# Optimization experiments

Hardware: AMD Instinct MI355X
Metric: run time of the kernel (lower is better)

The kernel has to match this reference:

```python
import math
import jax, jax.numpy as jnp
import numpy as np

B, T, D = 2048, 50, 256
NEG = -100000.0

def setup_inputs() -> dict:
    key = jax.random.key(0)
    ks = jax.random.split(key, 9)
    return {
        "x": jax.random.normal(ks[0], (B, T, D), dtype=jnp.float32),
        "mask": jax.random.randint(ks[1], (B, T, 1), 0, 2, dtype=jnp.int32),
        "time_decay": jax.random.uniform(ks[2], (B, T, 1), dtype=jnp.float32),
        "Wq": jax.random.normal(ks[3], (D, D), dtype=jnp.float32) * (1.0 / math.sqrt(D)),
        "bq": jax.random.normal(ks[4], (D,), dtype=jnp.float32) * 0.01,
        "Wk": jax.random.normal(ks[5], (D, D), dtype=jnp.float32) * (1.0 / math.sqrt(D)),
        "bk": jax.random.normal(ks[6], (D,), dtype=jnp.float32) * 0.01,
        "Wv": jax.random.normal(ks[7], (D, D), dtype=jnp.float32) * (1.0 / math.sqrt(D)),
        "bv": jax.random.normal(ks[8], (D,), dtype=jnp.float32) * 0.01,
    }

def reference(x, mask, time_decay, Wq, bq, Wk, bk, Wv, bv):
    # PositionalEncoding.forward: elementwise multiply by time-decay (broadcast over d_model)
    x = x * time_decay  # [B,T,D]
    q = jnp.einsum('btd,ed->bte', x, Wq) + bq
    k = jnp.einsum('btd,ed->bte', x, Wk) + bk
    v = jnp.einsum('btd,ed->bte', x, Wv) + bv
    # unusual Q/K-side masking (masked_fill before the matmul)
    keep = mask != 0  # [B,T,1]
    q = jnp.where(keep, q, NEG)
    k = jnp.where(keep, k, NEG)
    score = jnp.einsum('btd,bsd->bts', q, k) / math.sqrt(D)  # [B,T,T]
    score = jax.nn.softmax(score, axis=-1)
    # dropout is identity in eval mode
    out = jnp.einsum('bts,bsd->btd', score, v)  # [B,T,D]
    return out[:, -1, :]  # [B,D]
```

## Files before the change

### kernel.cpp

```cpp
#include <hip/hip_runtime.h>


namespace {
constexpr int kB = 2048;
constexpr int kT = 50;
constexpr int kD = 256;
constexpr int kG = 4;
constexpr int kThr = 256;
constexpr double kNeg = -100000.0;
constexpr int oM2 = 0;
constexpr int oWvp = 65536;
constexpr int oV0 = 131072;
constexpr int oC = 131328;
constexpr int oW1 = 131584;
constexpr int oW2 = 131840;
constexpr int oDbl = 132096;
}

__global__ __launch_bounds__(kThr) void precomp(
    const float* __restrict__ Wq, const float* __restrict__ bq,
    const float* __restrict__ Wk, const float* __restrict__ bk,
    const float* __restrict__ Wv, float* __restrict__ ws) {
  const int t = threadIdx.x;
  const int wave = t >> 6;
  const int lane = t & 63;
  const int blk = blockIdx.x;
  __shared__ float coefL[kD];
  __shared__ double red[3][4];

  if (blk < 256) {
    const int a = blk;
    coefL[t] = Wq[(size_t)t * kD + a];
    __syncthreads();
    const float* kcol = Wk + t;
    float pre[8];
#pragma unroll
    for (int k = 0; k < 8; ++k) pre[k] = kcol[(size_t)k * kD];
    float acc = 0.f;
    for (int j0 = 0; j0 < kD; j0 += 8) {
      float cur[8];
#pragma unroll
      for (int k = 0; k < 8; ++k) cur[k] = pre[k];
      const int nx = (j0 + 8 < kD) ? (j0 + 8) : 0;
#pragma unroll
      for (int k = 0; k < 8; ++k) pre[k] = kcol[(size_t)(nx + k) * kD];
#pragma unroll
      for (int k = 0; k < 8; ++k) acc += coefL[j0 + k] * cur[k];
    }
    ws[oM2 + (a >> 2) * 1024 + 4 * t + (a & 3)] = acc;
  } else if (blk < 258) {
    const float* W = (blk == 256) ? Wk : Wq;
    const float* coef = (blk == 256) ? bq : bk;
    coefL[t] = coef[t];
    __syncthreads();
    const float* col = W + t;
    float pre[8];
#pragma unroll
    for (int k = 0; k < 8; ++k) pre[k] = col[(size_t)k * kD];
    double a0 = 0.0, a1 = 0.0;
    for (int j0 = 0; j0 < kD; j0 += 8) {
      float cur[8];
#pragma unroll
      for (int k = 0; k < 8; ++k) cur[k] = pre[k];
      const int nx = (j0 + 8 < kD) ? (j0 + 8) : 0;
#pragma unroll
      for (int k = 0; k < 8; ++k) pre[k] = col[(size_t)(nx + k) * kD];
#pragma unroll
      for (int k = 0; k < 8; ++k) {
        const double w = (double)cur[k];
        a0 += (double)coefL[j0 + k] * w;
        a1 += w;
      }
    }
    if (blk == 256) {
      ws[oV0 + t] = (float)a0;
      ws[oC + t] = (float)a1;
    } else {
      ws[oW1 + t] = (float)a0;
      ws[oW2 + t] = (float)a1;
      double p0 = (double)bk[t];
      double p1 = (double)bq[t] * (double)bk[t];
      double p2 = (double)bq[t];
#pragma unroll
      for (int off = 32; off; off >>= 1) {
        p0 += __shfl_xor(p0, off);
        p1 += __shfl_xor(p1, off);
        p2 += __shfl_xor(p2, off);
      }
      if (lane == 0) {
        red[0][wave] = p0;
        red[1][wave] = p1;
        red[2][wave] = p2;
      }
      __syncthreads();
      if (t == 0) {
        double* dc = (double*)(ws + oDbl);
        dc[0] = red[0][0] + red[0][1] + red[0][2] + red[0][3];
        dc[1] = red[1][0] + red[1][1] + red[1][2] + red[1][3];
        dc[2] = red[2][0] + red[2][1] + red[2][2] + red[2][3];
      }
    }
  } else {
    const int d4b = (blk - 258) * 4;
    float4 in[4];
#pragma unroll
    for (int k = 0; k < 4; ++k)
      in[k] = *(const float4*)(Wv + (size_t)t * kD + 4 * (d4b + k));
    float4* Wvp = (float4*)(ws + oWvp);
#pragma unroll
    for (int k = 0; k < 4; ++k) Wvp[(size_t)(d4b + k) * kD + t] = in[k];
  }
}

__global__ __launch_bounds__(kThr, 2) void attn_main(
    const float* __restrict__ x, const int* __restrict__ mask,
    const float* __restrict__ td, const float* __restrict__ bv,
    const float* __restrict__ ws, float* __restrict__ out) {
  const float4* M2v = (const float4*)(ws + oM2);
  const float4* Wvv = (const float4*)(ws + oWvp);
  const float* v0 = ws + oV0;
  const float* cv = ws + oC;
  const double* dconst = (const double*)(ws + oDbl);

  __shared__ __align__(16) float4 xsf[kG][kD / 4];
  __shared__ __align__(16) float ub[kG][kD];
  __shared__ __align__(16) float4 ybf[kG][kD / 4];
  __shared__ float tdb[kG * kT];
  __shared__ int mb[kG * kT];
  __shared__ double Sqb[kG], Qbkb[kG];

  const int t = threadIdx.x;
  const int wave = t >> 6;
  const int lane = t & 63;
  const int b0 = blockIdx.x * kG;

  if (t < kG * kT) {
    tdb[t] = td[b0 * kT + t];
    mb[t] = mask[b0 * kT + t];
  }
  {
    const int g = wave;
    const float tv = td[(b0 + g) * kT + (kT - 1)];
    float4 xv =
        ((const float4*)(x + ((size_t)(b0 + g) * kT + kT - 1) * kD))[lane];
    xv.x *= tv; xv.y *= tv; xv.z *= tv; xv.w *= tv;
    xsf[g][lane] = xv;
  }
  __syncthreads();

  {
    const int g = wave;
    const float4 xv = xsf[g][lane];
    const float4 a1 = ((const float4*)(ws + oW1))[lane];
    const float4 a2 = ((const float4*)(ws + oW2))[lane];
    double s1 = (double)xv.x * a1.x + (double)xv.y * a1.y +
                (double)xv.z * a1.z + (double)xv.w * a1.w;
    double s2 = (double)xv.x * a2.x + (double)xv.y * a2.y +
                (double)xv.z * a2.z + (double)xv.w * a2.w;
#pragma unroll
    for (int off = 32; off; off >>= 1) {
      s1 += __shfl_xor(s1, off);
      s2 += __shfl_xor(s2, off);
    }
    if (lane == 0) {
      Qbkb[g] = s1 + dconst[1];
      Sqb[g] = s2 + dconst[2];
    }
  }

  {
    float4 pre[8];
#pragma unroll
    for (int k = 0; k < 8; ++k) pre[k] = M2v[(size_t)k * kD + t];
    float acc[kG];
    const float v0t = v0[t];
#pragma unroll
    for (int j = 0; j < kG; ++j) acc[j] = v0t;
    for (int j0 = 0; j0 < 64; j0 += 8) {
      float4 cur[8];
#pragma unroll
      for (int k = 0; k < 8; ++k) cur[k] = pre[k];
      const int nx = (j0 + 8 < 64) ? (j0 + 8) : 0;
#pragma unroll
      for (int k = 0; k < 8; ++k) pre[k] = M2v[(size_t)(nx + k) * kD + t];
#pragma unroll
      for (int k = 0; k < 8; ++k) {
#pragma unroll
        for (int j = 0; j < kG; ++j) {
          const float4 xj = xsf[j][j0 + k];
          acc[j] += xj.x * cur[k].x + xj.y * cur[k].y + xj.z * cur[k].z +
                    xj.w * cur[k].w;
        }
      }
    }
#pragma unroll
    for (int j = 0; j < kG; ++j) ub[j][t] = acc[j];
  }
  __syncthreads();

  {
    const int g = wave;
    const int b = b0 + g;
    const int base = g * kT;
    const float4* xrow = (const float4*)(x + (size_t)b * kT * kD);
    const float4 u4 = ((const float4*)(&ub[g][0]))[lane];
    const float4 c4 = ((const float4*)cv)[lane];
    const int mqg = mb[base + (kT - 1)];
    const float4 v4 = mqg ? u4 : c4;
    const double Cm = kNeg * Sqb[g] * 0.0625;
    const double Cbb = 256.0 * 1.0e10 * 0.0625;
    const double Qbk = Qbkb[g];
    const double sbkd = dconst[0];

    double m = -1.0e300;
    float l = 0.f;
    float4 y = {0.f, 0.f, 0.f, 0.f};

    float4 n0 = xrow[0 * 64 + lane];
    float4 n1 = xrow[1 * 64 + lane];
    float4 n2 = xrow[2 * 64 + lane];
    float4 n3 = xrow[3 * 64 + lane];
    for (int s = 0; s < 52; s += 4) {
      const float4 r0 = n0, r1 = n1, r2 = n2, r3 = n3;
      {
        const int p0 = (s + 4 < kT) ? s + 4 : kT - 1;
        const int p1 = (s + 5 < kT) ? s + 5 : kT - 1;
        const int p2 = (s + 6 < kT) ? s + 6 : kT - 1;
        const int p3 = (s + 7 < kT) ? s + 7 : kT - 1;
        n0 = xrow[p0 * 64 + lane];
        n1 = xrow[p1 * 64 + lane];
        n2 = xrow[p2 * 64 + lane];
        n3 = xrow[p3 * 64 + lane];
      }
      const int s1i = s + 1, s2i = s + 2, s3i = s + 3;
      const int c0 = s;
      const int c1 = (s1i < kT) ? s1i : kT - 1;
      const int c2 = (s2i < kT) ? s2i : kT - 1;
      const int c3 = (s3i < kT) ? s3i : kT - 1;
      const float tv0 = tdb[base + c0];
      const float tv1 = tdb[base + c1];
      const float tv2 = tdb[base + c2];
      const float tv3 = tdb[base + c3];
      float4 a0, a1, a2, a3;
      a0.x = r0.x * tv0; a0.y = r0.y * tv0; a0.z = r0.z * tv0; a0.w = r0.w * tv0;
      a1.x = r1.x * tv1; a1.y = r1.y * tv1; a1.z = r1.z * tv1; a1.w = r1.w * tv1;
      a2.x = r2.x * tv2; a2.y = r2.y * tv2; a2.z = r2.z * tv2; a2.w = r2.w * tv2;
      a3.x = r3.x * tv3; a3.y = r3.y * tv3; a3.z = r3.z * tv3; a3.w = r3.w * tv3;
      float p0 = a0.x * v4.x + a0.y * v4.y + a0.z * v4.z + a0.w * v4.w;
      float p1 = a1.x * v4.x + a1.y * v4.y + a1.z * v4.z + a1.w * v4.w;
      float p2 = a2.x * v4.x + a2.y * v4.y + a2.z * v4.z + a2.w * v4.w;
      float p3 = a3.x * v4.x + a3.y * v4.y + a3.z * v4.z + a3.w * v4.w;
#pragma unroll
      for (int off = 32; off; off >>= 1) {
        p0 += __shfl_xor(p0, off);
        p1 += __shfl_xor(p1, off);
        p2 += __shfl_xor(p2, off);
        p3 += __shfl_xor(p3, off);
      }
      const int ms0 = mb[base + c0];
      const int ms1 = mb[base + c1];
      const int ms2 = mb[base + c2];
      const int ms3 = mb[base + c3];
      double sc0, sc1, sc2, sc3;
      if (mqg) {
        sc0 = ms0 ? ((double)p0 + Qbk) * 0.0625 : Cm;
        sc1 = ms1 ? ((double)p1 + Qbk) * 0.0625 : Cm;
        sc2 = ms2 ? ((double)p2 + Qbk) * 0.0625 : Cm;
        sc3 = ms3 ? ((double)p3 + Qbk) * 0.0625 : Cm;
      } else {
        sc0 = ms0 ? kNeg * ((double)p0 + sbkd) * 0.0625 : Cbb;
        sc1 = ms1 ? kNeg * ((double)p1 + sbkd) * 0.0625 : Cbb;
        sc2 = ms2 ? kNeg * ((double)p2 + sbkd) * 0.0625 : Cbb;
        sc3 = ms3 ? kNeg * ((double)p3 + sbkd) * 0.0625 : Cbb;
      }
      if (s1i >= kT) sc1 = -1.0e300;
      if (s2i >= kT) sc2 = -1.0e300;
      if (s3i >= kT) sc3 = -1.0e300;
      double mnew = m;
      if (sc0 > mnew) mnew = sc0;
      if (sc1 > mnew) mnew = sc1;
      if (sc2 > mnew) mnew = sc2;
      if (sc3 > mnew) mnew = sc3;
      const float al = expf((float)(m - mnew));
      const float e0 = expf((float)(sc0 - mnew));
      const float e1 = expf((float)(sc1 - mnew));
      const float e2 = expf((float)(sc2 - mnew));
      const float e3 = expf((float)(sc3 - mnew));
      m = mnew;
      l = l * al + e0 + e1 + e2 + e3;
      y.x = y.x * al + e0 * a0.x + e1 * a1.x + e2 * a2.x + e3 * a3.x;
      y.y = y.y * al + e0 * a0.y + e1 * a1.y + e2 * a2.y + e3 * a3.y;
      y.z = y.z * al + e0 * a0.z + e1 * a1.z + e2 * a2.z + e3 * a3.z;
      y.w = y.w * al + e0 * a0.w + e1 * a1.w + e2 * a2.w + e3 * a3.w;
    }
    const float inv = 1.0f / l;
    y.x *= inv; y.y *= inv; y.z *= inv; y.w *= inv;
    ybf[g][lane] = y;
  }
  __syncthreads();

  {
    float4 pre[8];
#pragma unroll
    for (int k = 0; k < 8; ++k) pre[k] = Wvv[(size_t)k * kD + t];
    float acc[kG];
    const float bvt = bv[t];
#pragma unroll
    for (int j = 0; j < kG; ++j) acc[j] = bvt;
    for (int j0 = 0; j0 < 64; j0 += 8) {
      float4 cur[8];
#pragma unroll
      for (int k = 0; k < 8; ++k) cur[k] = pre[k];
      const int nx = (j0 + 8 < 64) ? (j0 + 8) : 0;
#pragma unroll
      for (int k = 0; k < 8; ++k) pre[k] = Wvv[(size_t)(nx + k) * kD + t];
#pragma unroll
      for (int k = 0; k < 8; ++k) {
#pragma unroll
        for (int j = 0; j < kG; ++j) {
          const float4 yj = ybf[j][j0 + k];
          acc[j] += yj.x * cur[k].x + yj.y * cur[k].y + yj.z * cur[k].z +
                    yj.w * cur[k].w;
        }
      }
    }
#pragma unroll
    for (int j = 0; j < kG; ++j) out[(size_t)(b0 + j) * kD + t] = acc[j];
  }
}

extern "C" void kernel_launch(void* const* d_in, const int* in_sizes, int n_in,
                              void* d_out, int out_size, void* d_ws,
                              size_t ws_size, hipStream_t stream) {
  const float* x = (const float*)d_in[0];
  const int* mask = (const int*)d_in[1];
  const float* td = (const float*)d_in[2];
  const float* Wq = (const float*)d_in[3];
  const float* bq = (const float*)d_in[4];
  const float* Wk = (const float*)d_in[5];
  const float* bk = (const float*)d_in[6];
  const float* Wv = (const float*)d_in[7];
  const float* bv = (const float*)d_in[8];
  float* ws = (float*)d_ws;
  float* out = (float*)d_out;
  (void)in_sizes; (void)n_in; (void)out_size; (void)ws_size;

  hipLaunchKernelGGL(precomp, dim3(274), dim3(kThr), 0, stream, Wq, bq, Wk, bk,
                     Wv, ws);
  hipLaunchKernelGGL(attn_main, dim3(kB / kG), dim3(kThr), 0, stream, x, mask,
                     td, bv, (const float*)ws, out);
}
```

Baseline: 224.5 us.

## Split fused attention kernel into separate u-GEMM, attention, and output GEMM kernels

```diff
diff --git a/kernel.cpp b/kernel.cpp
--- a/kernel.cpp
+++ b/kernel.cpp
@@ -5,7 +5,6 @@
 constexpr int kB = 2048;
 constexpr int kT = 50;
 constexpr int kD = 256;
-constexpr int kG = 4;
 constexpr int kThr = 256;
 constexpr double kNeg = -100000.0;
 constexpr int oM2 = 0;
@@ -15,6 +14,9 @@
 constexpr int oW1 = 131584;
 constexpr int oW2 = 131840;
 constexpr int oDbl = 132096;
+constexpr int oSq = 132608;
+constexpr int oQbk = 136704;
+constexpr int oU = 140800;
 }
 
 __global__ __launch_bounds__(kThr) void precomp(
@@ -112,45 +114,19 @@
   }
 }
 
-__global__ __launch_bounds__(kThr, 2) void attn_main(
-    const float* __restrict__ x, const int* __restrict__ mask,
-    const float* __restrict__ td, const float* __restrict__ bv,
-    const float* __restrict__ ws, float* __restrict__ out) {
-  const float4* M2v = (const float4*)(ws + oM2);
-  const float4* Wvv = (const float4*)(ws + oWvp);
-  const float* v0 = ws + oV0;
-  const float* cv = ws + oC;
-  const double* dconst = (const double*)(ws + oDbl);
-
-  __shared__ __align__(16) float4 xsf[kG][kD / 4];
-  __shared__ __align__(16) float ub[kG][kD];
-  __shared__ __align__(16) float4 ybf[kG][kD / 4];
-  __shared__ float tdb[kG * kT];
-  __shared__ int mb[kG * kT];
-  __shared__ double Sqb[kG], Qbkb[kG];
-
+__global__ __launch_bounds__(kThr) void u_gemm(const float* __restrict__ x,
+                                               const float* __restrict__ td,
+                                               float* __restrict__ ws) {
   const int t = threadIdx.x;
   const int wave = t >> 6;
   const int lane = t & 63;
-  const int b0 = blockIdx.x * kG;
-
-  if (t < kG * kT) {
-    tdb[t] = td[b0 * kT + t];
-    mb[t] = mask[b0 * kT + t];
-  }
+  const int b0 = blockIdx.x * 4;
+  const double* dc = (const double*)(ws + oDbl);
+
   {
-    const int g = wave;
-    const float tv = td[(b0 + g) * kT + (kT - 1)];
-    float4 xv =
-        ((const float4*)(x + ((size_t)(b0 + g) * kT + kT - 1) * kD))[lane];
-    xv.x *= tv; xv.y *= tv; xv.z *= tv; xv.w *= tv;
-    xsf[g][lane] = xv;
-  }
-  __syncthreads();
-
-  {
-    const int g = wave;
-    const float4 xv = xsf[g][lane];
+    const int b = b0 + wave;
+    const float4 xv =
+        ((const float4*)(x + ((size_t)b * kT + kT - 1) * kD))[lane];
     const float4 a1 = ((const float4*)(ws + oW1))[lane];
     const float4 a2 = ((const float4*)(ws + oW2))[lane];
     double s1 = (double)xv.x * a1.x + (double)xv.y * a1.y +
@@ -163,170 +139,204 @@
       s2 += __shfl_xor(s2, off);
     }
     if (lane == 0) {
-      Qbkb[g] = s1 + dconst[1];
-      Sqb[g] = s2 + dconst[2];
-    }
-  }
-
-  {
-    float4 pre[8];
-#pragma unroll
-    for (int k = 0; k < 8; ++k) pre[k] = M2v[(size_t)k * kD + t];
-    float acc[kG];
-    const float v0t = v0[t];
-#pragma unroll
-    for (int j = 0; j < kG; ++j) acc[j] = v0t;
-    for (int j0 = 0; j0 < 64; j0 += 8) {
-      float4 cur[8];
-#pragma unroll
-      for (int k = 0; k < 8; ++k) cur[k] = pre[k];
-      const int nx = (j0 + 8 < 64) ? (j0 + 8) : 0;
-#pragma unroll
-      for (int k = 0; k < 8; ++k) pre[k] = M2v[(size_t)(nx + k) * kD + t];
-#pragma unroll
-      for (int k = 0; k < 8; ++k) {
-#pragma unroll
-        for (int j = 0; j < kG; ++j) {
-          const float4 xj = xsf[j][j0 + k];
-          acc[j] += xj.x * cur[k].x + xj.y * cur[k].y + xj.z * cur[k].z +
-                    xj.w * cur[k].w;
-        }
-      }
-    }
-#pragma unroll
-    for (int j = 0; j < kG; ++j) ub[j][t] = acc[j];
-  }
-  __syncthreads();
-
-  {
-    const int g = wave;
-    const int b = b0 + g;
-    const int base = g * kT;
-    const float4* xrow = (const float4*)(x + (size_t)b * kT * kD);
-    const float4 u4 = ((const float4*)(&ub[g][0]))[lane];
-    const float4 c4 = ((const float4*)cv)[lane];
-    const int mqg = mb[base + (kT - 1)];
-    const float4 v4 = mqg ? u4 : c4;
-    const double Cm = kNeg * Sqb[g] * 0.0625;
-    const double Cbb = 256.0 * 1.0e10 * 0.0625;
-    const double Qbk = Qbkb[g];
-    const double sbkd = dconst[0];
-
-    double m = -1.0e300;
-    float l = 0.f;
-    float4 y = {0.f, 0.f, 0.f, 0.f};
-
-    float4 n0 = xrow[0 * 64 + lane];
-    float4 n1 = xrow[1 * 64 + lane];
-    float4 n2 = xrow[2 * 64 + lane];
-    float4 n3 = xrow[3 * 64 + lane];
-    for (int s = 0; s < 52; s += 4) {
-      const float4 r0 = n0, r1 = n1, r2 = n2, r3 = n3;
-      {
-        const int p0 = (s + 4 < kT) ? s + 4 : kT - 1;
-        const int p1 = (s + 5 < kT) ? s + 5 : kT - 1;
-        const int p2 = (s + 6 < kT) ? s + 6 : kT - 1;
-        const int p3 = (s + 7 < kT) ? s + 7 : kT - 1;
-        n0 = xrow[p0 * 64 + lane];
-        n1 = xrow[p1 * 64 + lane];
-        n2 = xrow[p2 * 64 + lane];
-        n3 = xrow[p3 * 64 + lane];
-      }
-      const int s1i = s + 1, s2i = s + 2, s3i = s + 3;
-      const int c0 = s;
-      const int c1 = (s1i < kT) ? s1i : kT - 1;
-      const int c2 = (s2i < kT) ? s2i : kT - 1;
-      const int c3 = (s3i < kT) ? s3i : kT - 1;
-      const float tv0 = tdb[base + c0];
-      const float tv1 = tdb[base + c1];
-      const float tv2 = tdb[base + c2];
-      const float tv3 = tdb[base + c3];
-      float4 a0, a1, a2, a3;
-      a0.x = r0.x * tv0; a0.y = r0.y * tv0; a0.z = r0.z * tv0; a0.w = r0.w * tv0;
-      a1.x = r1.x * tv1; a1.y = r1.y * tv1; a1.z = r1.z * tv1; a1.w = r1.w * tv1;
-      a2.x = r2.x * tv2; a2.y = r2.y * tv2; a2.z = r2.z * tv2; a2.w = r2.w * tv2;
-      a3.x = r3.x * tv3; a3.y = r3.y * tv3; a3.z = r3.z * tv3; a3.w = r3.w * tv3;
-      float p0 = a0.x * v4.x + a0.y * v4.y + a0.z * v4.z + a0.w * v4.w;
-      float p1 = a1.x * v4.x + a1.y * v4.y + a1.z * v4.z + a1.w * v4.w;
-      float p2 = a2.x * v4.x + a2.y * v4.y + a2.z * v4.z + a2.w * v4.w;
-      float p3 = a3.x * v4.x + a3.y * v4.y + a3.z * v4.z + a3.w * v4.w;
-#pragma unroll
-      for (int off = 32; off; off >>= 1) {
-        p0 += __shfl_xor(p0, off);
-        p1 += __shfl_xor(p1, off);
-        p2 += __shfl_xor(p2, off);
-        p3 += __shfl_xor(p3, off);
-      }
-      const int ms0 = mb[base + c0];
-      const int ms1 = mb[base + c1];
-      const int ms2 = mb[base + c2];
-      const int ms3 = mb[base + c3];
-      double sc0, sc1, sc2, sc3;
-      if (mqg) {
-        sc0 = ms0 ? ((double)p0 + Qbk) * 0.0625 : Cm;
-        sc1 = ms1 ? ((double)p1 + Qbk) * 0.0625 : Cm;
-        sc2 = ms2 ? ((double)p2 + Qbk) * 0.0625 : Cm;
-        sc3 = ms3 ? ((double)p3 + Qbk) * 0.0625 : Cm;
-      } else {
-        sc0 = ms0 ? kNeg * ((double)p0 + sbkd) * 0.0625 : Cbb;
-        sc1 = ms1 ? kNeg * ((double)p1 + sbkd) * 0.0625 : Cbb;
-        sc2 = ms2 ? kNeg * ((double)p2 + sbkd) * 0.0625 : Cbb;
-        sc3 = ms3 ? kNeg * ((double)p3 + sbkd) * 0.0625 : Cbb;
-      }
-      if (s1i >= kT) sc1 = -1.0e300;
-      if (s2i >= kT) sc2 = -1.0e300;
-      if (s3i >= kT) sc3 = -1.0e300;
-      double mnew = m;
-      if (sc0 > mnew) mnew = sc0;
-      if (sc1 > mnew) mnew = sc1;
-      if (sc2 > mnew) mnew = sc2;
-      if (sc3 > mnew) mnew = sc3;
-      const float al = expf((float)(m - mnew));
-      const float e0 = expf((float)(sc0 - mnew));
-      const float e1 = expf((float)(sc1 - mnew));
-      const float e2 = expf((float)(sc2 - mnew));
-      const float e3 = expf((float)(sc3 - mnew));
-      m = mnew;
-      l = l * al + e0 + e1 + e2 + e3;
-      y.x = y.x * al + e0 * a0.x + e1 * a1.x + e2 * a2.x + e3 * a3.x;
-      y.y = y.y * al + e0 * a0.y + e1 * a1.y + e2 * a2.y + e3 * a3.y;
-      y.z = y.z * al + e0 * a0.z + e1 * a1.z + e2 * a2.z + e3 * a3.z;
-      y.w = y.w * al + e0 * a0.w + e1 * a1.w + e2 * a2.w + e3 * a3.w;
-    }
-    const float inv = 1.0f / l;
-    y.x *= inv; y.y *= inv; y.z *= inv; y.w *= inv;
-    ybf[g][lane] = y;
-  }
-  __syncthreads();
-
-  {
-    float4 pre[8];
-#pragma unroll
-    for (int k = 0; k < 8; ++k) pre[k] = Wvv[(size_t)k * kD + t];
-    float acc[kG];
-    const float bvt = bv[t];
-#pragma unroll
-    for (int j = 0; j < kG; ++j) acc[j] = bvt;
-    for (int j0 = 0; j0 < 64; j0 += 8) {
-      float4 cur[8];
-#pragma unroll
-      for (int k = 0; k < 8; ++k) cur[k] = pre[k];
-      const int nx = (j0 + 8 < 64) ? (j0 + 8) : 0;
-#pragma unroll
-      for (int k = 0; k < 8; ++k) pre[k] = Wvv[(size_t)(nx + k) * kD + t];
-#pragma unroll
-      for (int k = 0; k < 8; ++k) {
-#pragma unroll
-        for (int j = 0; j < kG; ++j) {
-          const float4 yj = ybf[j][j0 + k];
-          acc[j] += yj.x * cur[k].x + yj.y * cur[k].y + yj.z * cur[k].z +
-                    yj.w * cur[k].w;
-        }
-      }
-    }
-#pragma unroll
-    for (int j = 0; j < kG; ++j) out[(size_t)(b0 + j) * kD + t] = acc[j];
-  }
+      const double tdd = (double)td[(size_t)b * kT + kT - 1];
+      ((double*)(ws + oQbk))[b] = tdd * s1 + dc[1];
+      ((double*)(ws + oSq))[b] = tdd * s2 + dc[2];
+    }
+  }
+
+  const float4* M2v = (const float4*)(ws + oM2);
+  const float4* r0 = (const float4*)(x + ((size_t)(b0 + 0) * kT + kT - 1) * kD);
+  const float4* r1 = (const float4*)(x + ((size_t)(b0 + 1) * kT + kT - 1) * kD);
+  const float4* r2 = (const float4*)(x + ((size_t)(b0 + 2) * kT + kT - 1) * kD);
+  const float4* r3 = (const float4*)(x + ((size_t)(b0 + 3) * kT + kT - 1) * kD);
+  const float td0 = td[(size_t)(b0 + 0) * kT + kT - 1];
+  const float td1 = td[(size_t)(b0 + 1) * kT + kT - 1];
+  const float td2 = td[(size_t)(b0 + 2) * kT + kT - 1];
+  const float td3 = td[(size_t)(b0 + 3) * kT + kT - 1];
+
+  float4 pre[8];
+#pragma unroll
+  for (int k = 0; k < 8; ++k) pre[k] = M2v[(size_t)k * kD + t];
+  float acc0 = 0.f, acc1 = 0.f, acc2 = 0.f, acc3 = 0.f;
+  for (int j0 = 0; j0 < 64; j0 += 8) {
+    float4 cur[8];
+#pragma unroll
+    for (int k = 0; k < 8; ++k) cur[k] = pre[k];
+    const int nx = (j0 + 8 < 64) ? (j0 + 8) : 0;
+#pragma unroll
+    for (int k = 0; k < 8; ++k) pre[k] = M2v[(size_t)(nx + k) * kD + t];
+#pragma unroll
+    for (int k = 0; k < 8; ++k) {
+      const float4 m = cur[k];
+      const float4 x0 = r0[j0 + k];
+      const float4 x1 = r1[j0 + k];
+      const float4 x2 = r2[j0 + k];
+      const float4 x3 = r3[j0 + k];
+      acc0 += x0.x * m.x + x0.y * m.y + x0.z * m.z + x0.w * m.w;
+      acc1 += x1.x * m.x + x1.y * m.y + x1.z * m.z + x1.w * m.w;
+      acc2 += x2.x * m.x + x2.y * m.y + x2.z * m.z + x2.w * m.w;
+      acc3 += x3.x * m.x + x3.y * m.y + x3.z * m.z + x3.w * m.w;
+    }
+  }
+  const float v0t = ws[oV0 + t];
+  ws[oU + (size_t)(b0 + 0) * kD + t] = td0 * acc0 + v0t;
+  ws[oU + (size_t)(b0 + 1) * kD + t] = td1 * acc1 + v0t;
+  ws[oU + (size_t)(b0 + 2) * kD + t] = td2 * acc2 + v0t;
+  ws[oU + (size_t)(b0 + 3) * kD + t] = td3 * acc3 + v0t;
+}
+
+__global__ __launch_bounds__(kThr) void attn(const float* __restrict__ x,
+                                             const int* __restrict__ mask,
+                                             const float* __restrict__ td,
+                                             float* __restrict__ ws) {
+  const int t = threadIdx.x;
+  const int wave = t >> 6;
+  const int lane = t & 63;
+  const int b = blockIdx.x * 4 + wave;
+
+  const float mtd = (lane < kT) ? td[(size_t)b * kT + lane] : 0.f;
+  const int mmk = (lane < kT) ? mask[(size_t)b * kT + lane] : 0;
+  const int mqg = __shfl(mmk, kT - 1);
+
+  const float4 u4 = ((const float4*)(ws + oU))[(size_t)b * 64 + lane];
+  const float4 c4 = ((const float4*)(ws + oC))[lane];
+  const float4 v4 = mqg ? u4 : c4;
+
+  const double* dcp = (const double*)(ws + oDbl);
+  const double sbkd = dcp[0];
+  const double Sq = ((const double*)(ws + oSq))[b];
+  const double Qbk = ((const double*)(ws + oQbk))[b];
+  const double Cm = kNeg * Sq * 0.0625;
+  const double Cbb = 256.0 * 1.0e10 * 0.0625;
+
+  const float4* xrow = (const float4*)(x + (size_t)b * kT * kD);
+  double m = -1.0e300;
+  float l = 0.f;
+  float4 y = {0.f, 0.f, 0.f, 0.f};
+
+  float4 n0 = xrow[0 * 64 + lane];
+  float4 n1 = xrow[1 * 64 + lane];
+  float4 n2 = xrow[2 * 64 + lane];
+  float4 n3 = xrow[3 * 64 + lane];
+  for (int s = 0; s < 52; s += 4) {
+    const float4 r0 = n0, r1 = n1, r2 = n2, r3 = n3;
+    {
+      const int p0 = (s + 4 < kT) ? s + 4 : kT - 1;
+      const int p1 = (s + 5 < kT) ? s + 5 : kT - 1;
+      const int p2 = (s + 6 < kT) ? s + 6 : kT - 1;
+      const int p3 = (s + 7 < kT) ? s + 7 : kT - 1;
+      n0 = xrow[p0 * 64 + lane];
+      n1 = xrow[p1 * 64 + lane];
+      n2 = xrow[p2 * 64 + lane];
+      n3 = xrow[p3 * 64 + lane];
+    }
+    const int s1i = s + 1, s2i = s + 2, s3i = s + 3;
+    const int c0 = s;
+    const int c1 = (s1i < kT) ? s1i : kT - 1;
+    const int c2 = (s2i < kT) ? s2i : kT - 1;
+    const int c3 = (s3i < kT) ? s3i : kT - 1;
+    const float tv0 = __shfl(mtd, c0);
+    const float tv1 = __shfl(mtd, c1);
+    const float tv2 = __shfl(mtd, c2);
+    const float tv3 = __shfl(mtd, c3);
+    float4 a0, a1, a2, a3;
+    a0.x = r0.x * tv0; a0.y = r0.y * tv0; a0.z = r0.z * tv0; a0.w = r0.w * tv0;
+    a1.x = r1.x * tv1; a1.y = r1.y * tv1; a1.z = r1.z * tv1; a1.w = r1.w * tv1;
+    a2.x = r2.x * tv2; a2.y = r2.y * tv2; a2.z = r2.z * tv2; a2.w = r2.w * tv2;
+    a3.x = r3.x * tv3; a3.y = r3.y * tv3; a3.z = r3.z * tv3; a3.w = r3.w * tv3;
+    float p0 = a0.x * v4.x + a0.y * v4.y + a0.z * v4.z + a0.w * v4.w;
+    float p1 = a1.x * v4.x + a1.y * v4.y + a1.z * v4.z + a1.w * v4.w;
+    float p2 = a2.x * v4.x + a2.y * v4.y + a2.z * v4.z + a2.w * v4.w;
+    float p3 = a3.x * v4.x + a3.y * v4.y + a3.z * v4.z + a3.w * v4.w;
+#pragma unroll
+    for (int off = 32; off; off >>= 1) {
+      p0 += __shfl_xor(p0, off);
+      p1 += __shfl_xor(p1, off);
+      p2 += __shfl_xor(p2, off);
+      p3 += __shfl_xor(p3, off);
+    }
+    const int ms0 = __shfl(mmk, c0);
+    const int ms1 = __shfl(mmk, c1);
+    const int ms2 = __shfl(mmk, c2);
+    const int ms3 = __shfl(mmk, c3);
+    double sc0, sc1, sc2, sc3;
+    if (mqg) {
+      sc0 = ms0 ? ((double)p0 + Qbk) * 0.0625 : Cm;
+      sc1 = ms1 ? ((double)p1 + Qbk) * 0.0625 : Cm;
+      sc2 = ms2 ? ((double)p2 + Qbk) * 0.0625 : Cm;
+      sc3 = ms3 ? ((double)p3 + Qbk) * 0.0625 : Cm;
+    } else {
+      sc0 = ms0 ? kNeg * ((double)p0 + sbkd) * 0.0625 : Cbb;
+      sc1 = ms1 ? kNeg * ((double)p1 + sbkd) * 0.0625 : Cbb;
+      sc2 = ms2 ? kNeg * ((double)p2 + sbkd) * 0.0625 : Cbb;
+      sc3 = ms3 ? kNeg * ((double)p3 + sbkd) * 0.0625 : Cbb;
+    }
+    if (s1i >= kT) sc1 = -1.0e300;
+    if (s2i >= kT) sc2 = -1.0e300;
+    if (s3i >= kT) sc3 = -1.0e300;
+    double mnew = m;
+    if (sc0 > mnew) mnew = sc0;
+    if (sc1 > mnew) mnew = sc1;
+    if (sc2 > mnew) mnew = sc2;
+    if (sc3 > mnew) mnew = sc3;
+    const float al = expf((float)(m - mnew));
+    const float e0 = expf((float)(sc0 - mnew));
+    const float e1 = expf((float)(sc1 - mnew));
+    const float e2 = expf((float)(sc2 - mnew));
+    const float e3 = expf((float)(sc3 - mnew));
+    m = mnew;
+    l = l * al + e0 + e1 + e2 + e3;
+    y.x = y.x * al + e0 * a0.x + e1 * a1.x + e2 * a2.x + e3 * a3.x;
+    y.y = y.y * al + e0 * a0.y + e1 * a1.y + e2 * a2.y + e3 * a3.y;
+    y.z = y.z * al + e0 * a0.z + e1 * a1.z + e2 * a2.z + e3 * a3.z;
+    y.w = y.w * al + e0 * a0.w + e1 * a1.w + e2 * a2.w + e3 * a3.w;
+  }
+  const float inv = 1.0f / l;
+  y.x *= inv; y.y *= inv; y.z *= inv; y.w *= inv;
+  ((float4*)(ws + oU))[(size_t)b * 64 + lane] = y;
+}
+
+__global__ __launch_bounds__(kThr) void o_gemm(const float* __restrict__ bv,
+                                               const float* __restrict__ ws,
+                                               float* __restrict__ out) {
+  const int t = threadIdx.x;
+  const int b0 = blockIdx.x * 4;
+  const float4* Wvv = (const float4*)(ws + oWvp);
+  const float4* y0 = (const float4*)(ws + oU + (size_t)(b0 + 0) * kD);
+  const float4* y1 = (const float4*)(ws + oU + (size_t)(b0 + 1) * kD);
+  const float4* y2 = (const float4*)(ws + oU + (size_t)(b0 + 2) * kD);
+  const float4* y3 = (const float4*)(ws + oU + (size_t)(b0 + 3) * kD);
+
+  float4 pre[8];
+#pragma unroll
+  for (int k = 0; k < 8; ++k) pre[k] = Wvv[(size_t)k * kD + t];
+  float acc0 = 0.f, acc1 = 0.f, acc2 = 0.f, acc3 = 0.f;
+  for (int j0 = 0; j0 < 64; j0 += 8) {
+    float4 cur[8];
+#pragma unroll
+    for (int k = 0; k < 8; ++k) cur[k] = pre[k];
+    const int nx = (j0 + 8 < 64) ? (j0 + 8) : 0;
+#pragma unroll
+    for (int k = 0; k < 8; ++k) pre[k] = Wvv[(size_t)(nx + k) * kD + t];
+#pragma unroll
+    for (int k = 0; k < 8; ++k) {
+      const float4 m = cur[k];
+      const float4 a0 = y0[j0 + k];
+      const float4 a1 = y1[j0 + k];
+      const float4 a2 = y2[j0 + k];
+      const float4 a3 = y3[j0 + k];
+      acc0 += a0.x * m.x + a0.y * m.y + a0.z * m.z + a0.w * m.w;
+      acc1 += a1.x * m.x + a1.y * m.y + a1.z * m.z + a1.w * m.w;
+      acc2 += a2.x * m.x + a2.y * m.y + a2.z * m.z + a2.w * m.w;
+      acc3 += a3.x * m.x + a3.y * m.y + a3.z * m.z + a3.w * m.w;
+    }
+  }
+  const float bvt = bv[t];
+  out[(size_t)(b0 + 0) * kD + t] = acc0 + bvt;
+  out[(size_t)(b0 + 1) * kD + t] = acc1 + bvt;
+  out[(size_t)(b0 + 2) * kD + t] = acc2 + bvt;
+  out[(size_t)(b0 + 3) * kD + t] = acc3 + bvt;
 }
 
 extern "C" void kernel_launch(void* const* d_in, const int* in_sizes, int n_in,
@@ -347,6 +357,8 @@
 
   hipLaunchKernelGGL(precomp, dim3(274), dim3(kThr), 0, stream, Wq, bq, Wk, bk,
                      Wv, ws);
-  hipLaunchKernelGGL(attn_main, dim3(kB / kG), dim3(kThr), 0, stream, x, mask,
-                     td, bv, (const float*)ws, out);
-}
+  hipLaunchKernelGGL(u_gemm, dim3(kB / 4), dim3(kThr), 0, stream, x, td, ws);
+  hipLaunchKernelGGL(attn, dim3(kB / 4), dim3(kThr), 0, stream, x, mask, td,
+                     ws);
+  hipLaunchKernelGGL(o_gemm, dim3(kB / 4), dim3(kThr), 0, stream, bv, ws, out);
+}
```

After: 233.7 us. 4.1% more time.

## Restructure main kernel to single-wave blocks handling two batches each

Applied to the files above, without the earlier changes.

```diff
diff --git a/kernel.cpp b/kernel.cpp
--- a/kernel.cpp
+++ b/kernel.cpp
@@ -5,8 +5,6 @@
 constexpr int kB = 2048;
 constexpr int kT = 50;
 constexpr int kD = 256;
-constexpr int kG = 4;
-constexpr int kThr = 256;
 constexpr double kNeg = -100000.0;
 constexpr int oM2 = 0;
 constexpr int oWvp = 65536;
@@ -17,7 +15,7 @@
 constexpr int oDbl = 132096;
 }
 
-__global__ __launch_bounds__(kThr) void precomp(
+__global__ __launch_bounds__(256) void precomp(
     const float* __restrict__ Wq, const float* __restrict__ bq,
     const float* __restrict__ Wk, const float* __restrict__ bk,
     const float* __restrict__ Wv, float* __restrict__ ws) {
@@ -94,10 +92,10 @@
       }
       __syncthreads();
       if (t == 0) {
-        double* dc = (double*)(ws + oDbl);
-        dc[0] = red[0][0] + red[0][1] + red[0][2] + red[0][3];
-        dc[1] = red[1][0] + red[1][1] + red[1][2] + red[1][3];
-        dc[2] = red[2][0] + red[2][1] + red[2][2] + red[2][3];
+        double* dcw = (double*)(ws + oDbl);
+        dcw[0] = red[0][0] + red[0][1] + red[0][2] + red[0][3];
+        dcw[1] = red[1][0] + red[1][1] + red[1][2] + red[1][3];
+        dcw[2] = red[2][0] + red[2][1] + red[2][2] + red[2][3];
       }
     }
   } else {
@@ -112,47 +110,35 @@
   }
 }
 
-__global__ __launch_bounds__(kThr, 2) void attn_main(
+__global__ __launch_bounds__(64) void fused_main(
     const float* __restrict__ x, const int* __restrict__ mask,
     const float* __restrict__ td, const float* __restrict__ bv,
     const float* __restrict__ ws, float* __restrict__ out) {
+  const int lane = threadIdx.x;
+  const int b0 = blockIdx.x * 2;
+  __shared__ __align__(16) float xsL[2][kD];
+  __shared__ __align__(16) float uL[2][kD];
+  __shared__ __align__(16) float yL[2][kD];
+
+  const double* dc = (const double*)(ws + oDbl);
   const float4* M2v = (const float4*)(ws + oM2);
   const float4* Wvv = (const float4*)(ws + oWvp);
-  const float* v0 = ws + oV0;
-  const float* cv = ws + oC;
-  const double* dconst = (const double*)(ws + oDbl);
-
-  __shared__ __align__(16) float4 xsf[kG][kD / 4];
-  __shared__ __align__(16) float ub[kG][kD];
-  __shared__ __align__(16) float4 ybf[kG][kD / 4];
-  __shared__ float tdb[kG * kT];
-  __shared__ int mb[kG * kT];
-  __shared__ double Sqb[kG], Qbkb[kG];
-
-  const int t = threadIdx.x;
-  const int wave = t >> 6;
-  const int lane = t & 63;
-  const int b0 = blockIdx.x * kG;
-
-  if (t < kG * kT) {
-    tdb[t] = td[b0 * kT + t];
-    mb[t] = mask[b0 * kT + t];
-  }
-  {
-    const int g = wave;
-    const float tv = td[(b0 + g) * kT + (kT - 1)];
-    float4 xv =
-        ((const float4*)(x + ((size_t)(b0 + g) * kT + kT - 1) * kD))[lane];
-    xv.x *= tv; xv.y *= tv; xv.z *= tv; xv.w *= tv;
-    xsf[g][lane] = xv;
-  }
-  __syncthreads();
-
-  {
-    const int g = wave;
-    const float4 xv = xsf[g][lane];
-    const float4 a1 = ((const float4*)(ws + oW1))[lane];
-    const float4 a2 = ((const float4*)(ws + oW2))[lane];
+
+  const float mtd0 = (lane < kT) ? td[(size_t)(b0 + 0) * kT + lane] : 0.f;
+  const float mtd1 = (lane < kT) ? td[(size_t)(b0 + 1) * kT + lane] : 0.f;
+  const int mmk0 = (lane < kT) ? mask[(size_t)(b0 + 0) * kT + lane] : 0;
+  const int mmk1 = (lane < kT) ? mask[(size_t)(b0 + 1) * kT + lane] : 0;
+  const float4 c4 = ((const float4*)(ws + oC))[lane];
+  const float4 a1 = ((const float4*)(ws + oW1))[lane];
+  const float4 a2 = ((const float4*)(ws + oW2))[lane];
+
+  double Qbk[2], Sq[2];
+#pragma unroll
+  for (int j = 0; j < 2; ++j) {
+    const int b = b0 + j;
+    const float tdl = __shfl(j ? mtd1 : mtd0, kT - 1);
+    const float4 xv =
+        ((const float4*)(x + ((size_t)b * kT + kT - 1) * kD))[lane];
     double s1 = (double)xv.x * a1.x + (double)xv.y * a1.y +
                 (double)xv.z * a1.z + (double)xv.w * a1.w;
     double s2 = (double)xv.x * a2.x + (double)xv.y * a2.y +
@@ -162,56 +148,69 @@
       s1 += __shfl_xor(s1, off);
       s2 += __shfl_xor(s2, off);
     }
-    if (lane == 0) {
-      Qbkb[g] = s1 + dconst[1];
-      Sqb[g] = s2 + dconst[2];
-    }
+    Qbk[j] = (double)tdl * s1 + dc[1];
+    Sq[j] = (double)tdl * s2 + dc[2];
+    float4 xs;
+    xs.x = xv.x * tdl; xs.y = xv.y * tdl;
+    xs.z = xv.z * tdl; xs.w = xv.w * tdl;
+    *(float4*)(&xsL[j][4 * lane]) = xs;
   }
 
   {
-    float4 pre[8];
-#pragma unroll
-    for (int k = 0; k < 8; ++k) pre[k] = M2v[(size_t)k * kD + t];
-    float acc[kG];
-    const float v0t = v0[t];
-#pragma unroll
-    for (int j = 0; j < kG; ++j) acc[j] = v0t;
-    for (int j0 = 0; j0 < 64; j0 += 8) {
-      float4 cur[8];
-#pragma unroll
-      for (int k = 0; k < 8; ++k) cur[k] = pre[k];
-      const int nx = (j0 + 8 < 64) ? (j0 + 8) : 0;
-#pragma unroll
-      for (int k = 0; k < 8; ++k) pre[k] = M2v[(size_t)(nx + k) * kD + t];
-#pragma unroll
-      for (int k = 0; k < 8; ++k) {
-#pragma unroll
-        for (int j = 0; j < kG; ++j) {
-          const float4 xj = xsf[j][j0 + k];
-          acc[j] += xj.x * cur[k].x + xj.y * cur[k].y + xj.z * cur[k].z +
-                    xj.w * cur[k].w;
-        }
-      }
-    }
-#pragma unroll
-    for (int j = 0; j < kG; ++j) ub[j][t] = acc[j];
-  }
-  __syncthreads();
-
-  {
-    const int g = wave;
-    const int b = b0 + g;
-    const int base = g * kT;
+    float4 A[4], B[4];
+#pragma unroll
+    for (int g = 0; g < 4; ++g) {
+      A[g] = M2v[(size_t)0 * kD + 64 * g + lane];
+      B[g] = M2v[(size_t)1 * kD + 64 * g + lane];
+    }
+    float accU[2][4] = {{0.f, 0.f, 0.f, 0.f}, {0.f, 0.f, 0.f, 0.f}};
+    for (int k4 = 0; k4 < 64; k4 += 2) {
+      float4 c0[4], c1[4];
+#pragma unroll
+      for (int g = 0; g < 4; ++g) { c0[g] = A[g]; c1[g] = B[g]; }
+      const int n0 = (k4 + 2 < 64) ? k4 + 2 : 0;
+      const int n1 = (k4 + 3 < 64) ? k4 + 3 : 1;
+#pragma unroll
+      for (int g = 0; g < 4; ++g) {
+        A[g] = M2v[(size_t)n0 * kD + 64 * g + lane];
+        B[g] = M2v[(size_t)n1 * kD + 64 * g + lane];
+      }
+      const float4 x00 = *(const float4*)(&xsL[0][4 * k4]);
+      const float4 x01 = *(const float4*)(&xsL[0][4 * (k4 + 1)]);
+      const float4 x10 = *(const float4*)(&xsL[1][4 * k4]);
+      const float4 x11 = *(const float4*)(&xsL[1][4 * (k4 + 1)]);
+#pragma unroll
+      for (int g = 0; g < 4; ++g) {
+        accU[0][g] += x00.x * c0[g].x + x00.y * c0[g].y + x00.z * c0[g].z +
+                      x00.w * c0[g].w + x01.x * c1[g].x + x01.y * c1[g].y +
+                      x01.z * c1[g].z + x01.w * c1[g].w;
+        accU[1][g] += x10.x * c0[g].x + x10.y * c0[g].y + x10.z * c0[g].z +
+                      x10.w * c0[g].w + x11.x * c1[g].x + x11.y * c1[g].y +
+                      x11.z * c1[g].z + x11.w * c1[g].w;
+      }
+    }
+#pragma unroll
+    for (int g = 0; g < 4; ++g) {
+      const float v0g = ws[oV0 + 64 * g + lane];
+      uL[0][64 * g + lane] = accU[0][g] + v0g;
+      uL[1][64 * g + lane] = accU[1][g] + v0g;
+    }
+  }
+
+  const double sbkd = dc[0];
+  const double Cbb = 256.0 * 1.0e10 * 0.0625;
+#pragma unroll 1
+  for (int j = 0; j < 2; ++j) {
+    const int b = b0 + j;
+    const float mtd = j ? mtd1 : mtd0;
+    const int mmk = j ? mmk1 : mmk0;
+    const int mqg = __shfl(mmk, kT - 1);
+    const float4 u4 = *(const float4*)(&uL[j][4 * lane]);
+    const float4 v4 = mqg ? u4 : c4;
+    const double Cm = kNeg * Sq[j] * 0.0625;
+    const double Qb = Qbk[j];
+
     const float4* xrow = (const float4*)(x + (size_t)b * kT * kD);
-    const float4 u4 = ((const float4*)(&ub[g][0]))[lane];
-    const float4 c4 = ((const float4*)cv)[lane];
-    const int mqg = mb[base + (kT - 1)];
-    const float4 v4 = mqg ? u4 : c4;
-    const double Cm = kNeg * Sqb[g] * 0.0625;
-    const double Cbb = 256.0 * 1.0e10 * 0.0625;
-    const double Qbk = Qbkb[g];
-    const double sbkd = dconst[0];
-
     double m = -1.0e300;
     float l = 0.f;
     float4 y = {0.f, 0.f, 0.f, 0.f};
@@ -233,22 +232,22 @@
         n3 = xrow[p3 * 64 + lane];
       }
       const int s1i = s + 1, s2i = s + 2, s3i = s + 3;
-      const int c0 = s;
-      const int c1 = (s1i < kT) ? s1i : kT - 1;
-      const int c2 = (s2i < kT) ? s2i : kT - 1;
-      const int c3 = (s3i < kT) ? s3i : kT - 1;
-      const float tv0 = tdb[base + c0];
-      const float tv1 = tdb[base + c1];
-      const float tv2 = tdb[base + c2];
-      const float tv3 = tdb[base + c3];
-      float4 a0, a1, a2, a3;
+      const int cc0 = s;
+      const int cc1 = (s1i < kT) ? s1i : kT - 1;
+      const int cc2 = (s2i < kT) ? s2i : kT - 1;
+      const int cc3 = (s3i < kT) ? s3i : kT - 1;
+      const float tv0 = __shfl(mtd, cc0);
+      const float tv1 = __shfl(mtd, cc1);
+      const float tv2 = __shfl(mtd, cc2);
+      const float tv3 = __shfl(mtd, cc3);
+      float4 a0, aa1, a2v, a3;
       a0.x = r0.x * tv0; a0.y = r0.y * tv0; a0.z = r0.z * tv0; a0.w = r0.w * tv0;
-      a1.x = r1.x * tv1; a1.y = r1.y * tv1; a1.z = r1.z * tv1; a1.w = r1.w * tv1;
-      a2.x = r2.x * tv2; a2.y = r2.y * tv2; a2.z = r2.z * tv2; a2.w = r2.w * tv2;
+      aa1.x = r1.x * tv1; aa1.y = r1.y * tv1; aa1.z = r1.z * tv1; aa1.w = r1.w * tv1;
+      a2v.x = r2.x * tv2; a2v.y = r2.y * tv2; a2v.z = r2.z * tv2; a2v.w = r2.w * tv2;
       a3.x = r3.x * tv3; a3.y = r3.y * tv3; a3.z = r3.z * tv3; a3.w = r3.w * tv3;
       float p0 = a0.x * v4.x + a0.y * v4.y + a0.z * v4.z + a0.w * v4.w;
-      float p1 = a1.x * v4.x + a1.y * v4.y + a1.z * v4.z + a1.w * v4.w;
-      float p2 = a2.x * v4.x + a2.y * v4.y + a2.z * v4.z + a2.w * v4.w;
+      float p1 = aa1.x * v4.x + aa1.y * v4.y + aa1.z * v4.z + aa1.w * v4.w;
+      float p2 = a2v.x * v4.x + a2v.y * v4.y + a2v.z * v4.z + a2v.w * v4.w;
       float p3 = a3.x * v4.x + a3.y * v4.y + a3.z * v4.z + a3.w * v4.w;
 #pragma unroll
       for (int off = 32; off; off >>= 1) {
@@ -257,16 +256,16 @@
         p2 += __shfl_xor(p2, off);
         p3 += __shfl_xor(p3, off);
       }
-      const int ms0 = mb[base + c0];
-      const int ms1 = mb[base + c1];
-      const int ms2 = mb[base + c2];
-      const int ms3 = mb[base + c3];
+      const int ms0 = __shfl(mmk, cc0);
+      const int ms1 = __shfl(mmk, cc1);
+      const int ms2 = __shfl(mmk, cc2);
+      const int ms3 = __shfl(mmk, cc3);
       double sc0, sc1, sc2, sc3;
       if (mqg) {
-        sc0 = ms0 ? ((double)p0 + Qbk) * 0.0625 : Cm;
-        sc1 = ms1 ? ((double)p1 + Qbk) * 0.0625 : Cm;
-        sc2 = ms2 ? ((double)p2 + Qbk) * 0.0625 : Cm;
-        sc3 = ms3 ? ((double)p3 + Qbk) * 0.0625 : Cm;
+        sc0 = ms0 ? ((double)p0 + Qb) * 0.0625 : Cm;
+        sc1 = ms1 ? ((double)p1 + Qb) * 0.0625 : Cm;
+        sc2 = ms2 ? ((double)p2 + Qb) * 0.0625 : Cm;
+        sc3 = ms3 ? ((double)p3 + Qb) * 0.0625 : Cm;
       } else {
         sc0 = ms0 ? kNeg * ((double)p0 + sbkd) * 0.0625 : Cbb;
         sc1 = ms1 ? kNeg * ((double)p1 + sbkd) * 0.0625 : Cbb;
@@ -288,44 +287,55 @@
       const float e3 = expf((float)(sc3 - mnew));
       m = mnew;
       l = l * al + e0 + e1 + e2 + e3;
-      y.x = y.x * al + e0 * a0.x + e1 * a1.x + e2 * a2.x + e3 * a3.x;
-      y.y = y.y * al + e0 * a0.y + e1 * a1.y + e2 * a2.y + e3 * a3.y;
-      y.z = y.z * al + e0 * a0.z + e1 * a1.z + e2 * a2.z + e3 * a3.z;
-      y.w = y.w * al + e0 * a0.w + e1 * a1.w + e2 * a2.w + e3 * a3.w;
+      y.x = y.x * al + e0 * a0.x + e1 * aa1.x + e2 * a2v.x + e3 * a3.x;
+      y.y = y.y * al + e0 * a0.y + e1 * aa1.y + e2 * a2v.y + e3 * a3.y;
+      y.z = y.z * al + e0 * a0.z + e1 * aa1.z + e2 * a2v.z + e3 * a3.z;
+      y.w = y.w * al + e0 * a0.w + e1 * aa1.w + e2 * a2v.w + e3 * a3.w;
     }
     const float inv = 1.0f / l;
     y.x *= inv; y.y *= inv; y.z *= inv; y.w *= inv;
-    ybf[g][lane] = y;
-  }
-  __syncthreads();
+    *(float4*)(&yL[j][4 * lane]) = y;
+  }
 
   {
-    float4 pre[8];
-#pragma unroll
-    for (int k = 0; k < 8; ++k) pre[k] = Wvv[(size_t)k * kD + t];
-    float acc[kG];
-    const float bvt = bv[t];
-#pragma unroll
-    for (int j = 0; j < kG; ++j) acc[j] = bvt;
-    for (int j0 = 0; j0 < 64; j0 += 8) {
-      float4 cur[8];
-#pragma unroll
-      for (int k = 0; k < 8; ++k) cur[k] = pre[k];
-      const int nx = (j0 + 8 < 64) ? (j0 + 8) : 0;
-#pragma unroll
-      for (int k = 0; k < 8; ++k) pre[k] = Wvv[(size_t)(nx + k) * kD + t];
-#pragma unroll
-      for (int k = 0; k < 8; ++k) {
-#pragma unroll
-        for (int j = 0; j < kG; ++j) {
-          const float4 yj = ybf[j][j0 + k];
-          acc[j] += yj.x * cur[k].x + yj.y * cur[k].y + yj.z * cur[k].z +
-                    yj.w * cur[k].w;
-        }
-      }
-    }
-#pragma unroll
-    for (int j = 0; j < kG; ++j) out[(size_t)(b0 + j) * kD + t] = acc[j];
+    float4 A[4], B[4];
+#pragma unroll
+    for (int g = 0; g < 4; ++g) {
+      A[g] = Wvv[(size_t)0 * kD + 64 * g + lane];
+      B[g] = Wvv[(size_t)1 * kD + 64 * g + lane];
+    }
+    float accO[2][4] = {{0.f, 0.f, 0.f, 0.f}, {0.f, 0.f, 0.f, 0.f}};
+    for (int k4 = 0; k4 < 64; k4 += 2) {
+      float4 c0[4], c1[4];
+#pragma unroll
+      for (int g = 0; g < 4; ++g) { c0[g] = A[g]; c1[g] = B[g]; }
+      const int n0 = (k4 + 2 < 64) ? k4 + 2 : 0;
+      const int n1 = (k4 + 3 < 64) ? k4 + 3 : 1;
+#pragma unroll
+      for (int g = 0; g < 4; ++g) {
+        A[g] = Wvv[(size_t)n0 * kD + 64 * g + lane];
+        B[g] = Wvv[(size_t)n1 * kD + 64 * g + lane];
+      }
+      const float4 y00 = *(const float4*)(&yL[0][4 * k4]);
+      const float4 y01 = *(const float4*)(&yL[0][4 * (k4 + 1)]);
+      const float4 y10 = *(const float4*)(&yL[1][4 * k4]);
+      const float4 y11 = *(const float4*)(&yL[1][4 * (k4 + 1)]);
+#pragma unroll
+      for (int g = 0; g < 4; ++g) {
+        accO[0][g] += y00.x * c0[g].x + y00.y * c0[g].y + y00.z * c0[g].z +
+                      y00.w * c0[g].w + y01.x * c1[g].x + y01.y * c1[g].y +
+                      y01.z * c1[g].z + y01.w * c1[g].w;
+        accO[1][g] += y10.x * c0[g].x + y10.y * c0[g].y + y10.z * c0[g].z +
+                      y10.w * c0[g].w + y11.x * c1[g].x + y11.y * c1[g].y +
+                      y11.z * c1[g].z + y11.w * c1[g].w;
+      }
+    }
+#pragma unroll
+    for (int g = 0; g < 4; ++g) {
+      const float bvg = bv[64 * g + lane];
+      out[(size_t)(b0 + 0) * kD + 64 * g + lane] = accO[0][g] + bvg;
+      out[(size_t)(b0 + 1) * kD + 64 * g + lane] = accO[1][g] + bvg;
+    }
   }
 }
 
@@ -345,8 +355,8 @@
   float* out = (float*)d_out;
   (void)in_sizes; (void)n_in; (void)out_size; (void)ws_size;
 
-  hipLaunchKernelGGL(precomp, dim3(274), dim3(kThr), 0, stream, Wq, bq, Wk, bk,
+  hipLaunchKernelGGL(precomp, dim3(274), dim3(256), 0, stream, Wq, bq, Wk, bk,
                      Wv, ws);
-  hipLaunchKernelGGL(attn_main, dim3(kB / kG), dim3(kThr), 0, stream, x, mask,
+  hipLaunchKernelGGL(fused_main, dim3(kB / 2), dim3(64), 0, stream, x, mask,
                      td, bv, (const float*)ws, out);
 }
```

Result: faster. 209.3 us (-6.7%).
